# Optimization experiments

Hardware: AMD Instinct MI355X
Metric: run time of the kernel (lower is better)

The kernel has to match this reference:

```python
import jax, jax.numpy as jnp
import numpy as np

NUM_HEADS = 8
HEAD_DIM = 64  # hidden_size 512 / 8 heads


def setup_inputs() -> dict:
    key = jax.random.key(0)
    ks = jax.random.split(key, 9)
    B, S, D, H = 64, 512, 512, 512  # batch, feat_num, input_size, hidden_size
    s = 0.02
    return {
        "x": jax.random.normal(ks[0], (B, S, D), dtype=jnp.float32),
        "wq": jax.random.normal(ks[1], (D, H), dtype=jnp.float32) * s,
        "bq": jax.random.normal(ks[2], (H,), dtype=jnp.float32) * s,
        "wk": jax.random.normal(ks[3], (D, H), dtype=jnp.float32) * s,
        "bk": jax.random.normal(ks[4], (H,), dtype=jnp.float32) * s,
        "wv": jax.random.normal(ks[5], (D, H), dtype=jnp.float32) * s,
        "bv": jax.random.normal(ks[6], (H,), dtype=jnp.float32) * s,
        "wo": jax.random.normal(ks[7], (H, D), dtype=jnp.float32) * s,
        "bo": jax.random.normal(ks[8], (D,), dtype=jnp.float32) * s,
    }


def reference(x, wq, bq, wk, bk, wv, bv, wo, bo):
    B, S, D = x.shape
    # QKV projections -> [B, heads, S, head_dim]
    def split_heads(t):
        return t.reshape(B, S, NUM_HEADS, HEAD_DIM).transpose(0, 2, 1, 3)
    q = split_heads(x @ wq + bq)
    k = split_heads(x @ wk + bk)
    v = split_heads(x @ wv + bv)
    # attention: [B, h, S, S]
    scores = jnp.einsum("bhsd,bhtd->bhst", q, k) / jnp.sqrt(
        jnp.asarray(HEAD_DIM, dtype=x.dtype)
    )
    probs = jax.nn.softmax(scores, axis=-1)  # dropout p=0 -> identity
    ctx = jnp.einsum("bhst,bhtd->bhsd", probs, v)
    ctx = ctx.transpose(0, 2, 1, 3).reshape(B, S, NUM_HEADS * HEAD_DIM)
    # output dense + residual + relu (dropout identity)
    out = jax.nn.relu(x + (ctx @ wo + bo))
    return out
```

## Files before the change

kernel.cpp:

```cpp
#include <hip/hip_runtime.h>
#include <hip/hip_bf16.h>

typedef unsigned short u16;
typedef __attribute__((ext_vector_type(8))) short short8;
typedef __attribute__((ext_vector_type(4))) float f32x4;

static __device__ __forceinline__ u16 f2b(float f) {
  unsigned u = __builtin_bit_cast(unsigned, f);
  unsigned r = u + 0x7fffu + ((u >> 16) & 1u);
  return (u16)(r >> 16);
}
static __device__ __forceinline__ unsigned pk2(float a, float b) {
  return (unsigned)f2b(a) | ((unsigned)f2b(b) << 16);
}

static __device__ __forceinline__ void gl_lds16(const u16* g, u16* l) {
  __builtin_amdgcn_global_load_lds(
      (const __attribute__((address_space(1))) unsigned*)g,
      (__attribute__((address_space(3))) unsigned*)l, 16, 0, 0);
}

__global__ __launch_bounds__(256) void prep_w(
    const float* __restrict__ wq, const float* __restrict__ wk,
    const float* __restrict__ wv, const float* __restrict__ wo,
    u16* __restrict__ wqkv_t, u16* __restrict__ wo_t) {
  int idx = blockIdx.x * 256 + threadIdx.x;
  if (idx < 512 * 1536) {
    int k = idx / 1536, n = idx % 1536;
    const float* w = (n < 512) ? wq : (n < 1024 ? wk : wv);
    wqkv_t[(size_t)n * 512 + k] = f2b(w[k * 512 + (n & 511)]);
  } else {
    int j = idx - 512 * 1536;
    int k = j >> 9, n = j & 511;
    wo_t[(size_t)n * 512 + k] = f2b(wo[k * 512 + n]);
  }
}

__global__ __launch_bounds__(256) void conv_x(const float* __restrict__ x,
                                              u16* __restrict__ xb) {
  int t = blockIdx.x * 256 + threadIdx.x;
  float4 v = *reinterpret_cast<const float4*>(&x[(size_t)t * 4]);
  uint2 p;
  p.x = pk2(v.x, v.y);
  p.y = pk2(v.z, v.w);
  *reinterpret_cast<uint2*>(&xb[(size_t)t * 4]) = p;
}

__global__ __launch_bounds__(256, 2) void gemm_qkv(
    const u16* __restrict__ xb, const u16* __restrict__ wt,
    const float* __restrict__ bq, const float* __restrict__ bk,
    const float* __restrict__ bv, u16* __restrict__ qkv) {
  __shared__ u16 As[128 * 64];
  __shared__ u16 Bs[128 * 64];
  const int tid = threadIdx.x;
  const int wave = tid >> 6, lane = tid & 63;
  const int wm = wave & 1, wn = wave >> 1;
  const int lr = lane & 15, lg = lane >> 4;
  const int m0 = blockIdx.x * 128, n0 = blockIdx.y * 128;

  const f32x4 fz = {0.f, 0.f, 0.f, 0.f};
  f32x4 acc[4][4];
#pragma unroll
  for (int i = 0; i < 4; ++i)
#pragma unroll
    for (int j = 0; j < 4; ++j) acc[i][j] = fz;

  for (int kb = 0; kb < 512; kb += 64) {
#pragma unroll
    for (int j = 0; j < 4; ++j) {
      const int cb = (wave * 4 + j) * 64;
      const int c = cb + lane;
      gl_lds16(&xb[(size_t)(m0 + (c >> 3)) * 512 + kb + ((c & 7) << 3)],
               &As[cb * 8]);
      gl_lds16(&wt[(size_t)(n0 + (c >> 3)) * 512 + kb + ((c & 7) << 3)],
               &Bs[cb * 8]);
    }
    __syncthreads();
#pragma unroll
    for (int ks = 0; ks < 2; ++ks) {
      short8 af[4], bb[4];
#pragma unroll
      for (int i = 0; i < 4; ++i)
        af[i] = *reinterpret_cast<const short8*>(
            &As[(wm * 64 + i * 16 + lr) * 64 + ks * 32 + lg * 8]);
#pragma unroll
      for (int j = 0; j < 4; ++j)
        bb[j] = *reinterpret_cast<const short8*>(
            &Bs[(wn * 64 + j * 16 + lr) * 64 + ks * 32 + lg * 8]);
#pragma unroll
      for (int i = 0; i < 4; ++i)
#pragma unroll
        for (int j = 0; j < 4; ++j)
          acc[i][j] = __builtin_amdgcn_mfma_f32_16x16x32_bf16(
              af[i], bb[j], acc[i][j], 0, 0, 0);
    }
    __syncthreads();
  }
#pragma unroll
  for (int i = 0; i < 4; ++i) {
    const int row0 = m0 + wm * 64 + i * 16 + lg * 4;
#pragma unroll
    for (int j = 0; j < 4; ++j) {
      const int col = n0 + wn * 64 + j * 16 + lr;
      const float bias =
          (col < 512) ? bq[col] : (col < 1024 ? bk[col - 512] : bv[col - 1024]);
#pragma unroll
      for (int r = 0; r < 4; ++r)
        qkv[(size_t)(row0 + r) * 1536 + col] = f2b(acc[i][j][r] + bias);
    }
  }
}

__global__ __launch_bounds__(256, 2) void attn(
    const u16* __restrict__ qkv, u16* __restrict__ ctx) {
  __shared__ u16 Qs[128 * 64];
  __shared__ u16 Ks[64 * 64];
  __shared__ u16 VsT[64 * 72];
  __shared__ u16 Ps[128 * 72];

  const int tid = threadIdx.x;
  const int wave = tid >> 6, lane = tid & 63;
  const int lr = lane & 15, lg = lane >> 4;
  const int bx = blockIdx.x;
  const int q0 = (bx & 3) * 128;
  const int h = (bx >> 2) & 7;
  const int b = bx >> 5;
  const size_t rowbase = (size_t)b * 512;
  const float scale = 0.125f;

#pragma unroll
  for (int j = 0; j < 4; ++j) {
    const int cb = (wave * 4 + j) * 64;
    const int c = cb + lane;
    gl_lds16(&qkv[(rowbase + q0 + (c >> 3)) * 1536 + h * 64 + ((c & 7) << 3)],
             &Qs[cb * 8]);
  }
  __syncthreads();
  short8 aq[2][2];
#pragma unroll
  for (int m = 0; m < 2; ++m)
#pragma unroll
    for (int ks = 0; ks < 2; ++ks)
      aq[m][ks] = *reinterpret_cast<const short8*>(
          &Qs[(wave * 32 + m * 16 + lr) * 64 + ks * 32 + lg * 8]);

  const f32x4 fz = {0.f, 0.f, 0.f, 0.f};
  f32x4 oacc[2][4];
#pragma unroll
  for (int m = 0; m < 2; ++m)
#pragma unroll
    for (int j = 0; j < 4; ++j) oacc[m][j] = fz;
  float lsum[2][4] = {{0.f, 0.f, 0.f, 0.f}, {0.f, 0.f, 0.f, 0.f}};

  for (int tt = 0; tt < 8; ++tt) {
    __syncthreads();
#pragma unroll
    for (int j = 0; j < 2; ++j) {
      const int cb = (wave * 2 + j) * 64;
      const int c = cb + lane;
      gl_lds16(
          &qkv[(rowbase + tt * 64 + (c >> 3)) * 1536 + 512 + h * 64 + ((c & 7) << 3)],
          &Ks[cb * 8]);
    }
#pragma unroll
    for (int i = 0; i < 2; ++i) {
      const int idx = tid + i * 256;
      const int r = idx >> 3, cg = idx & 7;
      uint4 v = *reinterpret_cast<const uint4*>(
          &qkv[(rowbase + tt * 64 + r) * 1536 + 1024 + h * 64 + cg * 8]);
      const u16* pv = reinterpret_cast<const u16*>(&v);
#pragma unroll
      for (int jj = 0; jj < 8; ++jj) VsT[(cg * 8 + jj) * 72 + r] = pv[jj];
    }
    __syncthreads();

    f32x4 st[2][4];
#pragma unroll
    for (int m = 0; m < 2; ++m)
#pragma unroll
      for (int j = 0; j < 4; ++j) st[m][j] = fz;
#pragma unroll
    for (int j = 0; j < 4; ++j) {
      short8 b0 = *reinterpret_cast<const short8*>(
          &Ks[(j * 16 + lr) * 64 + lg * 8]);
      short8 b1 = *reinterpret_cast<const short8*>(
          &Ks[(j * 16 + lr) * 64 + 32 + lg * 8]);
#pragma unroll
      for (int m = 0; m < 2; ++m) {
        st[m][j] =
            __builtin_amdgcn_mfma_f32_16x16x32_bf16(aq[m][0], b0, st[m][j], 0, 0, 0);
        st[m][j] =
            __builtin_amdgcn_mfma_f32_16x16x32_bf16(aq[m][1], b1, st[m][j], 0, 0, 0);
      }
    }

#pragma unroll
    for (int m = 0; m < 2; ++m)
#pragma unroll
      for (int j = 0; j < 4; ++j) {
#pragma unroll
        for (int r = 0; r < 4; ++r) {
          float e = __expf(st[m][j][r] * scale);
          st[m][j][r] = e;
          lsum[m][r] += e;
          Ps[(wave * 32 + m * 16 + lg * 4 + r) * 72 + j * 16 + lr] = f2b(e);
        }
      }

#pragma unroll
    for (int ks = 0; ks < 2; ++ks) {
      short8 ap[2];
#pragma unroll
      for (int m = 0; m < 2; ++m)
        ap[m] = *reinterpret_cast<const short8*>(
            &Ps[(wave * 32 + m * 16 + lr) * 72 + ks * 32 + lg * 8]);
#pragma unroll
      for (int jd = 0; jd < 4; ++jd) {
        short8 bv8 = *reinterpret_cast<const short8*>(
            &VsT[(jd * 16 + lr) * 72 + ks * 32 + lg * 8]);
#pragma unroll
        for (int m = 0; m < 2; ++m)
          oacc[m][jd] = __builtin_amdgcn_mfma_f32_16x16x32_bf16(
              ap[m], bv8, oacc[m][jd], 0, 0, 0);
      }
    }
  }

#pragma unroll
  for (int m = 0; m < 2; ++m)
#pragma unroll
    for (int r = 0; r < 4; ++r) {
      float s = lsum[m][r];
#pragma unroll
      for (int off = 1; off < 16; off <<= 1) s += __shfl_xor(s, off);
      lsum[m][r] = 1.0f / s;
    }
  const size_t coff = (rowbase + q0) * 512 + h * 64;
#pragma unroll
  for (int m = 0; m < 2; ++m)
#pragma unroll
    for (int jd = 0; jd < 4; ++jd) {
      const int dcol = jd * 16 + lr;
#pragma unroll
      for (int r = 0; r < 4; ++r) {
        const int row = wave * 32 + m * 16 + lg * 4 + r;
        ctx[coff + (size_t)row * 512 + dcol] = f2b(oacc[m][jd][r] * lsum[m][r]);
      }
    }
}

__global__ __launch_bounds__(256, 2) void gemm_out(
    const u16* __restrict__ ctx, const u16* __restrict__ wot,
    const float* __restrict__ x, const float* __restrict__ bo,
    float* __restrict__ out) {
  __shared__ u16 As[128 * 64];
  __shared__ u16 Bs[128 * 64];
  const int tid = threadIdx.x;
  const int wave = tid >> 6, lane = tid & 63;
  const int wm = wave & 1, wn = wave >> 1;
  const int lr = lane & 15, lg = lane >> 4;
  const int m0 = blockIdx.x * 128, n0 = blockIdx.y * 128;

  const f32x4 fz = {0.f, 0.f, 0.f, 0.f};
  f32x4 acc[4][4];
#pragma unroll
  for (int i = 0; i < 4; ++i)
#pragma unroll
    for (int j = 0; j < 4; ++j) acc[i][j] = fz;

  for (int kb = 0; kb < 512; kb += 64) {
#pragma unroll
    for (int j = 0; j < 4; ++j) {
      const int cb = (wave * 4 + j) * 64;
      const int c = cb + lane;
      gl_lds16(&ctx[(size_t)(m0 + (c >> 3)) * 512 + kb + ((c & 7) << 3)],
               &As[cb * 8]);
      gl_lds16(&wot[(size_t)(n0 + (c >> 3)) * 512 + kb + ((c & 7) << 3)],
               &Bs[cb * 8]);
    }
    __syncthreads();
#pragma unroll
    for (int ks = 0; ks < 2; ++ks) {
      short8 af[4], bb[4];
#pragma unroll
      for (int i = 0; i < 4; ++i)
        af[i] = *reinterpret_cast<const short8*>(
            &As[(wm * 64 + i * 16 + lr) * 64 + ks * 32 + lg * 8]);
#pragma unroll
      for (int j = 0; j < 4; ++j)
        bb[j] = *reinterpret_cast<const short8*>(
            &Bs[(wn * 64 + j * 16 + lr) * 64 + ks * 32 + lg * 8]);
#pragma unroll
      for (int i = 0; i < 4; ++i)
#pragma unroll
        for (int j = 0; j < 4; ++j)
          acc[i][j] = __builtin_amdgcn_mfma_f32_16x16x32_bf16(
              af[i], bb[j], acc[i][j], 0, 0, 0);
    }
    __syncthreads();
  }
#pragma unroll
  for (int i = 0; i < 4; ++i) {
#pragma unroll
    for (int j = 0; j < 4; ++j) {
      const int col = n0 + wn * 64 + j * 16 + lr;
#pragma unroll
      for (int r = 0; r < 4; ++r) {
        const int row = m0 + wm * 64 + i * 16 + lg * 4 + r;
        float v = acc[i][j][r] + bo[col] + x[(size_t)row * 512 + col];
        out[(size_t)row * 512 + col] = fmaxf(v, 0.0f);
      }
    }
  }
}

extern "C" void kernel_launch(void* const* d_in, const int* in_sizes, int n_in,
                              void* d_out, int out_size, void* d_ws,
                              size_t ws_size, hipStream_t stream) {
  const float* x = (const float*)d_in[0];
  const float* wq = (const float*)d_in[1];
  const float* bq = (const float*)d_in[2];
  const float* wk = (const float*)d_in[3];
  const float* bk = (const float*)d_in[4];
  const float* wv = (const float*)d_in[5];
  const float* bv = (const float*)d_in[6];
  const float* wo = (const float*)d_in[7];
  const float* bo = (const float*)d_in[8];
  float* out = (float*)d_out;

  char* ws = (char*)d_ws;
  u16* qkv = (u16*)ws;
  u16* ctx = (u16*)(ws + 100663296);
  u16* xb = ctx;
  u16* wqkv_t = (u16*)(ws + 134217728);
  u16* wo_t = (u16*)(ws + 135790592);

  hipLaunchKernelGGL(prep_w, dim3(4096), dim3(256), 0, stream, wq, wk, wv, wo,
                     wqkv_t, wo_t);
  hipLaunchKernelGGL(conv_x, dim3(16384), dim3(256), 0, stream, x, xb);
  hipLaunchKernelGGL(gemm_qkv, dim3(256, 12), dim3(256), 0, stream, xb, wqkv_t,
                     bq, bk, bv, qkv);
  hipLaunchKernelGGL(attn, dim3(2048), dim3(256), 0, stream, qkv, ctx);
  hipLaunchKernelGGL(gemm_out, dim3(256, 4), dim3(256), 0, stream, ctx, wo_t,
                     x, bo, out);
}
```

Before: 347.3 us.

## Double-buffer K/V in attention, keep P in registers, fuse prep kernels

Merges the weight transpose and the x-to-bf16 conversion into one prep launch. The Q projection now has the 1/sqrt(d) scale folded in, and V is written as fp16. The attention kernel computes S transposed so the exp'd probabilities stay in registers as fp16 MFMA operands, which removes the Ps LDS round trip. K and V loads are double-buffered with prefetch of the next tile, so one barrier per iteration replaces two. The context tile is staged through LDS so the global stores are coalesced 16-byte writes. Launch bounds rise to 3 blocks per CU. The fp16 V and P lose range compared with bf16, and the higher occupancy target may cause register spills.

```diff
diff --git a/kernel.cpp b/kernel.cpp
--- a/kernel.cpp
+++ b/kernel.cpp
@@ -2,8 +2,10 @@
 #include <hip/hip_bf16.h>
 
 typedef unsigned short u16;
+typedef unsigned int u32;
 typedef __attribute__((ext_vector_type(8))) short short8;
 typedef __attribute__((ext_vector_type(4))) float f32x4;
+typedef __attribute__((ext_vector_type(4))) _Float16 f16x4;
 
 static __device__ __forceinline__ u16 f2b(float f) {
   unsigned u = __builtin_bit_cast(unsigned, f);
@@ -13,6 +15,9 @@
 static __device__ __forceinline__ unsigned pk2(float a, float b) {
   return (unsigned)f2b(a) | ((unsigned)f2b(b) << 16);
 }
+static __device__ __forceinline__ u32 pkh(float a, float b) {
+  return __builtin_bit_cast(u32, __builtin_amdgcn_cvt_pkrtz(a, b));
+}
 
 static __device__ __forceinline__ void gl_lds16(const u16* g, u16* l) {
   __builtin_amdgcn_global_load_lds(
@@ -20,33 +25,31 @@
       (__attribute__((address_space(3))) unsigned*)l, 16, 0, 0);
 }
 
-__global__ __launch_bounds__(256) void prep_w(
+__global__ __launch_bounds__(256) void prep(
     const float* __restrict__ wq, const float* __restrict__ wk,
     const float* __restrict__ wv, const float* __restrict__ wo,
-    u16* __restrict__ wqkv_t, u16* __restrict__ wo_t) {
-  int idx = blockIdx.x * 256 + threadIdx.x;
-  if (idx < 512 * 1536) {
-    int k = idx / 1536, n = idx % 1536;
+    const float* __restrict__ x, u16* __restrict__ wqkv_t,
+    u16* __restrict__ wo_t, u16* __restrict__ xb) {
+  int t = blockIdx.x * 256 + threadIdx.x;
+  if (t < 786432) {
+    int k = t / 1536, n = t % 1536;
     const float* w = (n < 512) ? wq : (n < 1024 ? wk : wv);
     wqkv_t[(size_t)n * 512 + k] = f2b(w[k * 512 + (n & 511)]);
-  } else {
-    int j = idx - 512 * 1536;
+  } else if (t < 1048576) {
+    int j = t - 786432;
     int k = j >> 9, n = j & 511;
     wo_t[(size_t)n * 512 + k] = f2b(wo[k * 512 + n]);
-  }
-}
-
-__global__ __launch_bounds__(256) void conv_x(const float* __restrict__ x,
-                                              u16* __restrict__ xb) {
-  int t = blockIdx.x * 256 + threadIdx.x;
-  float4 v = *reinterpret_cast<const float4*>(&x[(size_t)t * 4]);
-  uint2 p;
-  p.x = pk2(v.x, v.y);
-  p.y = pk2(v.z, v.w);
-  *reinterpret_cast<uint2*>(&xb[(size_t)t * 4]) = p;
-}
-
-__global__ __launch_bounds__(256, 2) void gemm_qkv(
+  } else {
+    size_t i = (size_t)(t - 1048576) * 4;
+    float4 v = *reinterpret_cast<const float4*>(&x[i]);
+    uint2 p;
+    p.x = pk2(v.x, v.y);
+    p.y = pk2(v.z, v.w);
+    *reinterpret_cast<uint2*>(&xb[i]) = p;
+  }
+}
+
+__global__ __launch_bounds__(256, 3) void gemm_qkv(
     const u16* __restrict__ xb, const u16* __restrict__ wt,
     const float* __restrict__ bq, const float* __restrict__ bk,
     const float* __restrict__ bv, u16* __restrict__ qkv) {
@@ -105,18 +108,26 @@
       const float bias =
           (col < 512) ? bq[col] : (col < 1024 ? bk[col - 512] : bv[col - 1024]);
 #pragma unroll
-      for (int r = 0; r < 4; ++r)
-        qkv[(size_t)(row0 + r) * 1536 + col] = f2b(acc[i][j][r] + bias);
-    }
-  }
-}
-
-__global__ __launch_bounds__(256, 2) void attn(
-    const u16* __restrict__ qkv, u16* __restrict__ ctx) {
-  __shared__ u16 Qs[128 * 64];
-  __shared__ u16 Ks[64 * 64];
-  __shared__ u16 VsT[64 * 72];
-  __shared__ u16 Ps[128 * 72];
+      for (int r = 0; r < 4; ++r) {
+        float v = acc[i][j][r] + bias;
+        u16 ov;
+        if (col < 512)
+          ov = f2b(v * 0.125f);
+        else if (col < 1024)
+          ov = f2b(v);
+        else
+          ov = __builtin_bit_cast(u16, (_Float16)v);
+        qkv[(size_t)(row0 + r) * 1536 + col] = ov;
+      }
+    }
+  }
+}
+
+__global__ __launch_bounds__(256, 3) void attn(const u16* __restrict__ qkv,
+                                               u16* __restrict__ ctx) {
+  __shared__ u16 QOs[128 * 66];
+  __shared__ u16 Ks[2][64 * 64];
+  __shared__ u16 VsT[2][64 * 66];
 
   const int tid = threadIdx.x;
   const int wave = tid >> 6, lane = tid & 63;
@@ -126,130 +137,165 @@
   const int h = (bx >> 2) & 7;
   const int b = bx >> 5;
   const size_t rowbase = (size_t)b * 512;
-  const float scale = 0.125f;
 
 #pragma unroll
   for (int j = 0; j < 4; ++j) {
-    const int cb = (wave * 4 + j) * 64;
-    const int c = cb + lane;
+    const int cb = (wave * 4 + j) * 64, c = cb + lane;
     gl_lds16(&qkv[(rowbase + q0 + (c >> 3)) * 1536 + h * 64 + ((c & 7) << 3)],
-             &Qs[cb * 8]);
+             &QOs[cb * 8]);
+  }
+#pragma unroll
+  for (int j = 0; j < 2; ++j) {
+    const int cb = (wave * 2 + j) * 64, c = cb + lane;
+    gl_lds16(&qkv[(rowbase + (c >> 3)) * 1536 + 512 + h * 64 + ((c & 7) << 3)],
+             &Ks[0][cb * 8]);
+  }
+  uint4 vreg[2];
+#pragma unroll
+  for (int i = 0; i < 2; ++i) {
+    int idx = tid + i * 256, r = idx >> 3, cg = idx & 7;
+    vreg[i] = *reinterpret_cast<const uint4*>(
+        &qkv[(rowbase + r) * 1536 + 1024 + h * 64 + cg * 8]);
+  }
+#pragma unroll
+  for (int i = 0; i < 2; ++i) {
+    int idx = tid + i * 256, r = idx >> 3, cg = idx & 7;
+    const u16* pv = reinterpret_cast<const u16*>(&vreg[i]);
+#pragma unroll
+    for (int jj = 0; jj < 8; ++jj) VsT[0][(cg * 8 + jj) * 66 + r] = pv[jj];
   }
   __syncthreads();
+
   short8 aq[2][2];
 #pragma unroll
-  for (int m = 0; m < 2; ++m)
+  for (int g = 0; g < 2; ++g)
 #pragma unroll
     for (int ks = 0; ks < 2; ++ks)
-      aq[m][ks] = *reinterpret_cast<const short8*>(
-          &Qs[(wave * 32 + m * 16 + lr) * 64 + ks * 32 + lg * 8]);
+      aq[g][ks] = *reinterpret_cast<const short8*>(
+          &QOs[(wave * 32 + g * 16 + lr) * 64 + ks * 32 + lg * 8]);
 
   const f32x4 fz = {0.f, 0.f, 0.f, 0.f};
   f32x4 oacc[2][4];
 #pragma unroll
-  for (int m = 0; m < 2; ++m)
-#pragma unroll
-    for (int j = 0; j < 4; ++j) oacc[m][j] = fz;
-  float lsum[2][4] = {{0.f, 0.f, 0.f, 0.f}, {0.f, 0.f, 0.f, 0.f}};
+  for (int g = 0; g < 2; ++g)
+#pragma unroll
+    for (int dt = 0; dt < 4; ++dt) oacc[g][dt] = fz;
+  float lsum[2] = {0.f, 0.f};
 
   for (int tt = 0; tt < 8; ++tt) {
-    __syncthreads();
-#pragma unroll
-    for (int j = 0; j < 2; ++j) {
-      const int cb = (wave * 2 + j) * 64;
-      const int c = cb + lane;
-      gl_lds16(
-          &qkv[(rowbase + tt * 64 + (c >> 3)) * 1536 + 512 + h * 64 + ((c & 7) << 3)],
-          &Ks[cb * 8]);
-    }
-#pragma unroll
-    for (int i = 0; i < 2; ++i) {
-      const int idx = tid + i * 256;
-      const int r = idx >> 3, cg = idx & 7;
-      uint4 v = *reinterpret_cast<const uint4*>(
-          &qkv[(rowbase + tt * 64 + r) * 1536 + 1024 + h * 64 + cg * 8]);
-      const u16* pv = reinterpret_cast<const u16*>(&v);
-#pragma unroll
-      for (int jj = 0; jj < 8; ++jj) VsT[(cg * 8 + jj) * 72 + r] = pv[jj];
-    }
-    __syncthreads();
+    const int buf = tt & 1;
+    if (tt < 7) {
+#pragma unroll
+      for (int j = 0; j < 2; ++j) {
+        const int cb = (wave * 2 + j) * 64, c = cb + lane;
+        gl_lds16(&qkv[(rowbase + (tt + 1) * 64 + (c >> 3)) * 1536 + 512 +
+                      h * 64 + ((c & 7) << 3)],
+                 &Ks[buf ^ 1][cb * 8]);
+      }
+#pragma unroll
+      for (int i = 0; i < 2; ++i) {
+        int idx = tid + i * 256, r = idx >> 3, cg = idx & 7;
+        vreg[i] = *reinterpret_cast<const uint4*>(
+            &qkv[(rowbase + (tt + 1) * 64 + r) * 1536 + 1024 + h * 64 + cg * 8]);
+      }
+    }
 
     f32x4 st[2][4];
 #pragma unroll
-    for (int m = 0; m < 2; ++m)
-#pragma unroll
-      for (int j = 0; j < 4; ++j) st[m][j] = fz;
-#pragma unroll
-    for (int j = 0; j < 4; ++j) {
-      short8 b0 = *reinterpret_cast<const short8*>(
-          &Ks[(j * 16 + lr) * 64 + lg * 8]);
-      short8 b1 = *reinterpret_cast<const short8*>(
-          &Ks[(j * 16 + lr) * 64 + 32 + lg * 8]);
-#pragma unroll
-      for (int m = 0; m < 2; ++m) {
-        st[m][j] =
-            __builtin_amdgcn_mfma_f32_16x16x32_bf16(aq[m][0], b0, st[m][j], 0, 0, 0);
-        st[m][j] =
-            __builtin_amdgcn_mfma_f32_16x16x32_bf16(aq[m][1], b1, st[m][j], 0, 0, 0);
-      }
-    }
-
-#pragma unroll
-    for (int m = 0; m < 2; ++m)
-#pragma unroll
-      for (int j = 0; j < 4; ++j) {
-#pragma unroll
-        for (int r = 0; r < 4; ++r) {
-          float e = __expf(st[m][j][r] * scale);
-          st[m][j][r] = e;
-          lsum[m][r] += e;
-          Ps[(wave * 32 + m * 16 + lg * 4 + r) * 72 + j * 16 + lr] = f2b(e);
-        }
-      }
-
-#pragma unroll
-    for (int ks = 0; ks < 2; ++ks) {
-      short8 ap[2];
-#pragma unroll
-      for (int m = 0; m < 2; ++m)
-        ap[m] = *reinterpret_cast<const short8*>(
-            &Ps[(wave * 32 + m * 16 + lr) * 72 + ks * 32 + lg * 8]);
-#pragma unroll
-      for (int jd = 0; jd < 4; ++jd) {
-        short8 bv8 = *reinterpret_cast<const short8*>(
-            &VsT[(jd * 16 + lr) * 72 + ks * 32 + lg * 8]);
-#pragma unroll
-        for (int m = 0; m < 2; ++m)
-          oacc[m][jd] = __builtin_amdgcn_mfma_f32_16x16x32_bf16(
-              ap[m], bv8, oacc[m][jd], 0, 0, 0);
-      }
-    }
-  }
-
-#pragma unroll
-  for (int m = 0; m < 2; ++m)
-#pragma unroll
-    for (int r = 0; r < 4; ++r) {
-      float s = lsum[m][r];
-#pragma unroll
-      for (int off = 1; off < 16; off <<= 1) s += __shfl_xor(s, off);
-      lsum[m][r] = 1.0f / s;
-    }
+    for (int g = 0; g < 2; ++g)
+#pragma unroll
+      for (int mt = 0; mt < 4; ++mt) st[g][mt] = fz;
+#pragma unroll
+    for (int mt = 0; mt < 4; ++mt) {
+      short8 k0 = *reinterpret_cast<const short8*>(
+          &Ks[buf][(mt * 16 + lr) * 64 + lg * 8]);
+      short8 k1 = *reinterpret_cast<const short8*>(
+          &Ks[buf][(mt * 16 + lr) * 64 + 32 + lg * 8]);
+#pragma unroll
+      for (int g = 0; g < 2; ++g) {
+        st[g][mt] = __builtin_amdgcn_mfma_f32_16x16x32_bf16(k0, aq[g][0],
+                                                            st[g][mt], 0, 0, 0);
+        st[g][mt] = __builtin_amdgcn_mfma_f32_16x16x32_bf16(k1, aq[g][1],
+                                                            st[g][mt], 0, 0, 0);
+      }
+    }
+
+    f16x4 pfrag[2][4];
+#pragma unroll
+    for (int g = 0; g < 2; ++g)
+#pragma unroll
+      for (int mt = 0; mt < 4; ++mt) {
+        float e0 = __expf(st[g][mt][0]), e1 = __expf(st[g][mt][1]);
+        float e2 = __expf(st[g][mt][2]), e3 = __expf(st[g][mt][3]);
+        lsum[g] += (e0 + e1) + (e2 + e3);
+        uint2 uu;
+        uu.x = pkh(e0, e1);
+        uu.y = pkh(e2, e3);
+        pfrag[g][mt] = __builtin_bit_cast(f16x4, uu);
+      }
+
+#pragma unroll
+    for (int dt = 0; dt < 4; ++dt) {
+#pragma unroll
+      for (int tw = 0; tw < 4; ++tw) {
+        const int a0 = (dt * 16 + lr) * 66 + tw * 16 + lg * 4;
+        uint2 uu;
+        uu.x = *reinterpret_cast<const u32*>(&VsT[buf][a0]);
+        uu.y = *reinterpret_cast<const u32*>(&VsT[buf][a0 + 2]);
+        f16x4 vf = __builtin_bit_cast(f16x4, uu);
+#pragma unroll
+        for (int g = 0; g < 2; ++g)
+          oacc[g][dt] = __builtin_amdgcn_mfma_f32_16x16x16f16(
+              vf, pfrag[g][tw], oacc[g][dt], 0, 0, 0);
+      }
+    }
+
+    if (tt < 7) {
+#pragma unroll
+      for (int i = 0; i < 2; ++i) {
+        int idx = tid + i * 256, r = idx >> 3, cg = idx & 7;
+        const u16* pv = reinterpret_cast<const u16*>(&vreg[i]);
+#pragma unroll
+        for (int jj = 0; jj < 8; ++jj)
+          VsT[buf ^ 1][(cg * 8 + jj) * 66 + r] = pv[jj];
+      }
+    }
+    __syncthreads();
+  }
+
+#pragma unroll
+  for (int g = 0; g < 2; ++g) {
+    float s = lsum[g];
+    s += __shfl_xor(s, 16);
+    s += __shfl_xor(s, 32);
+    lsum[g] = 1.0f / s;
+  }
+#pragma unroll
+  for (int g = 0; g < 2; ++g)
+#pragma unroll
+    for (int dt = 0; dt < 4; ++dt) {
+      f32x4 o = oacc[g][dt];
+      const float li = lsum[g];
+      const int base = (wave * 32 + g * 16 + lr) * 66 + dt * 16 + lg * 4;
+      *reinterpret_cast<u32*>(&QOs[base]) = pk2(o[0] * li, o[1] * li);
+      *reinterpret_cast<u32*>(&QOs[base + 2]) = pk2(o[2] * li, o[3] * li);
+    }
+  __syncthreads();
   const size_t coff = (rowbase + q0) * 512 + h * 64;
 #pragma unroll
-  for (int m = 0; m < 2; ++m)
-#pragma unroll
-    for (int jd = 0; jd < 4; ++jd) {
-      const int dcol = jd * 16 + lr;
-#pragma unroll
-      for (int r = 0; r < 4; ++r) {
-        const int row = wave * 32 + m * 16 + lg * 4 + r;
-        ctx[coff + (size_t)row * 512 + dcol] = f2b(oacc[m][jd][r] * lsum[m][r]);
-      }
-    }
-}
-
-__global__ __launch_bounds__(256, 2) void gemm_out(
+  for (int i = 0; i < 4; ++i) {
+    int idx = tid + i * 256, r = idx >> 3, cg = idx & 7;
+    const u16* src = &QOs[r * 66 + cg * 8];
+    uint4 w;
+    w.x = *reinterpret_cast<const u32*>(&src[0]);
+    w.y = *reinterpret_cast<const u32*>(&src[2]);
+    w.z = *reinterpret_cast<const u32*>(&src[4]);
+    w.w = *reinterpret_cast<const u32*>(&src[6]);
+    *reinterpret_cast<uint4*>(&ctx[coff + (size_t)r * 512 + cg * 8]) = w;
+  }
+}
+
+__global__ __launch_bounds__(256, 3) void gemm_out(
     const u16* __restrict__ ctx, const u16* __restrict__ wot,
     const float* __restrict__ x, const float* __restrict__ bo,
     float* __restrict__ out) {
@@ -335,9 +381,8 @@
   u16* wqkv_t = (u16*)(ws + 134217728);
   u16* wo_t = (u16*)(ws + 135790592);
 
-  hipLaunchKernelGGL(prep_w, dim3(4096), dim3(256), 0, stream, wq, wk, wv, wo,
-                     wqkv_t, wo_t);
-  hipLaunchKernelGGL(conv_x, dim3(16384), dim3(256), 0, stream, x, xb);
+  hipLaunchKernelGGL(prep, dim3(20480), dim3(256), 0, stream, wq, wk, wv, wo,
+                     x, wqkv_t, wo_t, xb);
   hipLaunchKernelGGL(gemm_qkv, dim3(256, 12), dim3(256), 0, stream, xb, wqkv_t,
                      bq, bk, bv, qkv);
   hipLaunchKernelGGL(attn, dim3(2048), dim3(256), 0, stream, qkv, ctx);
```

After: 313.2 us. 1.11x faster.
